# Optimization experiments

Hardware: AMD Instinct MI355X
Metric: run time of the kernel (lower is better)

## Reference

```python
import jax, jax.numpy as jnp
import numpy as np

B, S, D, L, V, H, FF = 128, 256, 512, 4, 96, 8, 512
DH = D // H
EPS = 1e-3  # keras BatchNormalization default epsilon


def setup_inputs() -> dict:
    key = jax.random.key(0)
    ks = jax.random.split(key, 12)
    s = 0.02
    inp = {
        "sequence": jax.random.randint(ks[0], (B, S), 0, V),
        "pos_encodings": jax.random.normal(ks[1], (S, D), jnp.float32) * s,
        "embed": jax.random.normal(ks[2], (V, D), jnp.float32) * s,
        "Wq": jax.random.normal(ks[3], (L, D, D), jnp.float32) * s,
        "bq": jnp.zeros((L, D), jnp.float32),
        "Wk": jax.random.normal(ks[4], (L, D, D), jnp.float32) * s,
        "bk": jnp.zeros((L, D), jnp.float32),
        "Wv": jax.random.normal(ks[5], (L, D, D), jnp.float32) * s,
        "bv": jnp.zeros((L, D), jnp.float32),
        "Wo": jax.random.normal(ks[6], (L, D, D), jnp.float32) * s,
        "bo": jnp.zeros((L, D), jnp.float32),
        "gamma1": jnp.ones((L, D), jnp.float32),
        "beta1": jnp.zeros((L, D), jnp.float32),
        "W1": jax.random.normal(ks[7], (L, D, FF), jnp.float32) * s,
        "b1": jnp.zeros((L, FF), jnp.float32),
        "W2": jax.random.normal(ks[8], (L, FF, D), jnp.float32) * s,
        "b2": jnp.zeros((L, D), jnp.float32),
        "gamma2": jnp.ones((L, D), jnp.float32),
        "beta2": jnp.zeros((L, D), jnp.float32),
    }
    return inp


def _batchnorm(h, g, b):
    # training-mode BN over (batch, seq) per feature, eps=1e-3
    mu = jnp.mean(h, axis=(0, 1), keepdims=True)
    var = jnp.mean(jnp.square(h - mu), axis=(0, 1), keepdims=True)
    return (h - mu) * jax.lax.rsqrt(var + EPS) * g + b


def _encoder(sequence, pos_encodings, embed, layer_params):
    x = embed[sequence] + pos_encodings[None]  # [B,S,D]

    def layer(h, p):
        wq, bq_, wk, bk_, wv, bv_, wo, bo_, g1, be1, w1, bb1, w2, bb2, g2, be2 = p
        b_, s_, d_ = h.shape
        q = (h @ wq + bq_).reshape(b_, s_, H, DH)
        k = (h @ wk + bk_).reshape(b_, s_, H, DH)
        v = (h @ wv + bv_).reshape(b_, s_, H, DH)
        scores = jnp.einsum('bqhd,bkhd->bhqk', q, k) / jnp.sqrt(jnp.float32(DH))
        attn = jnp.einsum('bhqk,bkhd->bqhd', jax.nn.softmax(scores, axis=-1), v)
        attn = attn.reshape(b_, s_, d_) @ wo + bo_
        h = _batchnorm(h + attn, g1, be1)
        ffn = jax.nn.relu(h @ w1 + bb1) @ w2 + bb2
        h = _batchnorm(h + ffn, g2, be2)
        return h, None

    out, _ = jax.lax.scan(layer, x, layer_params)
    return out


def reference(sequence, pos_encodings, embed, Wq, bq, Wk, bk, Wv, bv, Wo, bo,
              gamma1, beta1, W1, b1, W2, b2, gamma2, beta2):
    layer_params = (Wq, bq, Wk, bk, Wv, bv, Wo, bo,
                    gamma1, beta1, W1, b1, W2, b2, gamma2, beta2)
    return _encoder(sequence, pos_encodings, embed, layer_params)
```

## Files before the change

### kernel.cpp

```cpp
#include <hip/hip_runtime.h>

#define B_   128
#define S_   256
#define D_   512
#define L_   4
#define H_   8
#define DH_  64
#define FF_  512
#define M_   32768
#define EPS_ 1e-3f

typedef unsigned short u16;
typedef unsigned int   u32;
typedef __bf16 bf16_8 __attribute__((ext_vector_type(8)));
typedef float  f32_4  __attribute__((ext_vector_type(4)));

__device__ __forceinline__ float bf2f(u16 u) {
  union { u32 i; float f; } x; x.i = ((u32)u) << 16; return x.f;
}
__device__ __forceinline__ u16 f2bf(float f) {
  union { float f; u32 i; } x; x.f = f;
  u32 r = x.i + 0x7fffu + ((x.i >> 16) & 1u);
  return (u16)(r >> 16);
}
__device__ __forceinline__ void async_cp16(const void* g, void* l) {
  __builtin_amdgcn_global_load_lds(
      (const __attribute__((address_space(1))) void*)g,
      (__attribute__((address_space(3))) void*)l, 16, 0, 0);
}

__global__ __launch_bounds__(256) void k_embed(const int* __restrict__ seq,
    const float* __restrict__ pos, const float* __restrict__ emb,
    u16* __restrict__ h)
{
  int t = blockIdx.x * 256 + threadIdx.x;
  int row = t >> 6;
  int c = (t & 63) * 8;
  int s = row & (S_ - 1);
  int tok = seq[row];
  const float* ep = emb + (size_t)tok * D_ + c;
  const float* pp = pos + (size_t)s * D_ + c;
  float4 e0 = *(const float4*)ep;
  float4 e1 = *(const float4*)(ep + 4);
  float4 p0 = *(const float4*)pp;
  float4 p1 = *(const float4*)(pp + 4);
  u32 o[4];
  o[0] = (u32)f2bf(e0.x + p0.x) | ((u32)f2bf(e0.y + p0.y) << 16);
  o[1] = (u32)f2bf(e0.z + p0.z) | ((u32)f2bf(e0.w + p0.w) << 16);
  o[2] = (u32)f2bf(e1.x + p1.x) | ((u32)f2bf(e1.y + p1.y) << 16);
  o[3] = (u32)f2bf(e1.z + p1.z) | ((u32)f2bf(e1.w + p1.w) << 16);
  *(uint4*)&h[(size_t)row * D_ + c] = make_uint4(o[0], o[1], o[2], o[3]);
}

__global__ __launch_bounds__(256) void k_transpose(
    const float* __restrict__ Wq, const float* __restrict__ Wk, const float* __restrict__ Wv,
    const float* __restrict__ Wo, const float* __restrict__ W1, const float* __restrict__ W2,
    u16* __restrict__ Wt)
{
  __shared__ u16 tile[32][33];
  int mat = blockIdx.z;
  int layer = mat / 6, w = mat % 6;
  const float* src = (w == 0) ? Wq : (w == 1) ? Wk : (w == 2) ? Wv
                   : (w == 3) ? Wo : (w == 4) ? W1 : W2;
  src += (size_t)layer * (D_ * D_);
  u16* dst = Wt + (size_t)mat * (D_ * D_);
  int bx = blockIdx.x * 32;
  int by = blockIdx.y * 32;
  int tx = threadIdx.x & 31, ty = threadIdx.x >> 5;
#pragma unroll
  for (int i = 0; i < 32; i += 8)
    tile[ty + i][tx] = f2bf(src[(size_t)(by + ty + i) * D_ + bx + tx]);
  __syncthreads();
#pragma unroll
  for (int i = 0; i < 32; i += 8)
    dst[(size_t)(bx + ty + i) * D_ + by + tx] = tile[tx][ty + i];
}

__global__ __launch_bounds__(256) void k_packbias(const float* __restrict__ bq,
    const float* __restrict__ bk, const float* __restrict__ bv, float* __restrict__ dst)
{
  int t = blockIdx.x * 256 + threadIdx.x;
  int l = t / 1536, j = t - l * 1536;
  const float* src = (j < 512) ? bq : (j < 1024) ? bk : bv;
  dst[t] = src[l * 512 + (j & 511)];
}

__global__ __launch_bounds__(256) void k_gemm(
    const u16* __restrict__ A, const u16* __restrict__ Bt,
    const float* __restrict__ bias, const u16* __restrict__ resid,
    u16* __restrict__ outb, float* __restrict__ stats,
    int mode)
{
  __shared__ __align__(16) u16 smem[24576];
  u16* As = smem;
  u16* Bs = smem + 12288;
  int tid = threadIdx.x;
  int m0 = blockIdx.y * 128;
  int n0 = blockIdx.x * 128;
  int w = tid >> 6, lane = tid & 63;
  int wm = (w >> 1) * 64, wn = (w & 1) * 64;
  int fr = lane & 15, lk = lane >> 4;

  int srow = lane >> 2;
  int schunk = (lane & 3) ^ ((lane >> 4) & 3);
  const u16* Ag0 = A  + (size_t)(m0 + w * 32 + srow) * 512 + schunk * 8;
  const u16* Ag1 = Ag0 + (size_t)16 * 512;
  const u16* Bg0 = Bt + (size_t)(n0 + w * 32 + srow) * 512 + schunk * 8;
  const u16* Bg1 = Bg0 + (size_t)16 * 512;
  int off0 = (w * 32) * 32;
  int off1 = (w * 32 + 16) * 32;

  f32_4 acc[4][4] = {};
  int ach = (lk ^ ((fr >> 2) & 3)) * 8;

  async_cp16(Ag0, &As[off0]);
  async_cp16(Ag1, &As[off1]);
  async_cp16(Bg0, &Bs[off0]);
  async_cp16(Bg1, &Bs[off1]);
  async_cp16(Ag0 + 32, &As[4096 + off0]);
  async_cp16(Ag1 + 32, &As[4096 + off1]);
  async_cp16(Bg0 + 32, &Bs[4096 + off0]);
  async_cp16(Bg1 + 32, &Bs[4096 + off1]);

#pragma unroll
  for (int it = 0; it < 16; it++) {
    if (it < 15) asm volatile("s_waitcnt vmcnt(4)" ::: "memory");
    else         asm volatile("s_waitcnt vmcnt(0)" ::: "memory");
    __builtin_amdgcn_s_barrier();
    asm volatile("" ::: "memory");
    if (it < 14) {
      int kn = (it + 2) * 32;
      int pn = ((it + 2) % 3) * 4096;
      async_cp16(Ag0 + kn, &As[pn + off0]);
      async_cp16(Ag1 + kn, &As[pn + off1]);
      async_cp16(Bg0 + kn, &Bs[pn + off0]);
      async_cp16(Bg1 + kn, &Bs[pn + off1]);
    }
    const u16* Ab = &As[(it % 3) * 4096];
    const u16* Bb = &Bs[(it % 3) * 4096];
    bf16_8 afr[4], bfr[4];
#pragma unroll
    for (int i = 0; i < 4; i++) {
      afr[i] = *(const bf16_8*)&Ab[(wm + i * 16 + fr) * 32 + ach];
      bfr[i] = *(const bf16_8*)&Bb[(wn + i * 16 + fr) * 32 + ach];
    }
#pragma unroll
    for (int i = 0; i < 4; i++)
#pragma unroll
      for (int j = 0; j < 4; j++)
        acc[i][j] = __builtin_amdgcn_mfma_f32_16x16x32_bf16(afr[i], bfr[j], acc[i][j], 0, 0, 0);
  }

  __syncthreads();
  u16* Ct = smem;
  int rbase = lk * 4;
#pragma unroll
  for (int j = 0; j < 4; j++) {
    int colin = wn + j * 16 + fr;
    int colg  = n0 + colin;
    float bv = bias[colg];
    float csum = 0.f, csq = 0.f;
#pragma unroll
    for (int i = 0; i < 4; i++) {
      int rowl = wm + i * 16 + rbase;
#pragma unroll
      for (int r = 0; r < 4; r++) {
        float c = acc[i][j][r] + bv;
        if (mode == 1) c = fmaxf(c, 0.f);
        if (mode == 2) {
          c += bf2f(resid[(size_t)(m0 + rowl + r) * 512 + colg]);
          csum += c; csq = fmaf(c, c, csq);
        }
        int rw = rowl + r;
        Ct[rw * 128 + (((colin >> 3) ^ (rw & 15)) << 3) + (colin & 7)] = f2bf(c);
      }
    }
    if (mode == 2) {
      csum += __shfl_xor(csum, 16); csum += __shfl_xor(csum, 32);
      csq  += __shfl_xor(csq, 16);  csq  += __shfl_xor(csq, 32);
      if (lk == 0) {
        atomicAdd(&stats[colg], csum);
        atomicAdd(&stats[512 + colg], csq);
      }
    }
  }
  __syncthreads();

#pragma unroll
  for (int rd = 0; rd < 8; rd++) {
    int lrow = w * 32 + rd * 4 + (lane >> 4);
    int s = lane & 15;
    uint4 val = *(const uint4*)&Ct[lrow * 128 + s * 8];
    int chunk = s ^ (lrow & 15);
    int grow = m0 + lrow;
    if (mode == 3) {
      int colg = n0 + chunk * 8;
      int cc = colg & 511;
      size_t idx = (size_t)(colg >> 9) * ((size_t)M_ * D_)
                 + ((size_t)((grow >> 8) * 8 + (cc >> 6)) * 256 + (grow & 255)) * 64 + (cc & 63);
      *(uint4*)&outb[idx] = val;
    } else {
      *(uint4*)&outb[(size_t)grow * 512 + n0 + chunk * 8] = val;
    }
  }
}

__global__ __launch_bounds__(256) void k_attn(
    const u16* __restrict__ q, const u16* __restrict__ k,
    const u16* __restrict__ v, u16* __restrict__ attn)
{
  __shared__ u16 Vt[64 * 256];
  __shared__ u16 Pm[4][16 * 64];
  int tid = threadIdx.x;
  int h = blockIdx.x & 7, b = blockIdx.x >> 3;
  size_t hb = (size_t)(b * 8 + h) * (256 * 64);
  int w = tid >> 6, lane = tid & 63;

  {
    int kp = tid & 127;
    int o  = tid >> 7;
    const u16* vp = v + hb + (size_t)(2 * kp) * 64 + o * 32;
    union { uint4 u[4]; u16 s[32]; } r0, r1;
#pragma unroll
    for (int i = 0; i < 4; i++) {
      r0.u[i] = *(const uint4*)(vp + i * 8);
      r1.u[i] = *(const uint4*)(vp + 64 + i * 8);
    }
#pragma unroll
    for (int d = 0; d < 32; d++) {
      int da = o * 32 + d;
      u32 val = (u32)r0.s[d] | ((u32)r1.s[d] << 16);
      int idx = da * 256 + ((((kp >> 2) ^ (da & 31)) << 3)) + ((2 * kp) & 7);
      *(u32*)&Vt[idx] = val;
    }
  }
  __syncthreads();

  int fr = lane & 15;
  int lk = lane >> 4;
  int rbase = lk * 4;
  const u16* kb = k + hb;

#pragma unroll 1
  for (int qt = 0; qt < 4; qt++) {
    int q0 = qt * 64 + w * 16;

    f32_4 accS[16];
    const u16* qbase = q + hb + (size_t)(q0 + fr) * 64 + lk * 8;
    bf16_8 af0 = *(const bf16_8*)(qbase);
    bf16_8 af1 = *(const bf16_8*)(qbase + 32);
    __builtin_amdgcn_s_setprio(1);
#pragma unroll
    for (int j = 0; j < 16; j++) {
      const u16* kr = kb + (size_t)(j * 16 + fr) * 64;
      bf16_8 bf0 = *(const bf16_8*)(kr + lk * 8);
      bf16_8 bf1 = *(const bf16_8*)(kr + 32 + lk * 8);
      f32_4 z = {};
      z = __builtin_amdgcn_mfma_f32_16x16x32_bf16(af0, bf0, z, 0, 0, 0);
      accS[j] = __builtin_amdgcn_mfma_f32_16x16x32_bf16(af1, bf1, z, 0, 0, 0);
    }
    __builtin_amdgcn_s_setprio(0);

    float l[4];
#pragma unroll
    for (int r = 0; r < 4; r++) {
      float m = accS[0][r];
#pragma unroll
      for (int j = 1; j < 16; j++) m = fmaxf(m, accS[j][r]);
      m = fmaxf(m, __shfl_xor(m, 1));
      m = fmaxf(m, __shfl_xor(m, 2));
      m = fmaxf(m, __shfl_xor(m, 4));
      m = fmaxf(m, __shfl_xor(m, 8));
      float s = 0.f;
#pragma unroll
      for (int j = 0; j < 16; j++) {
        float p = __expf((accS[j][r] - m) * 0.125f);
        accS[j][r] = p;
        s += p;
      }
      s += __shfl_xor(s, 1);
      s += __shfl_xor(s, 2);
      s += __shfl_xor(s, 4);
      s += __shfl_xor(s, 8);
      l[r] = s;
    }

    f32_4 accO[4] = {};
#pragma unroll
    for (int hs = 0; hs < 4; hs++) {
#pragma unroll
      for (int j4 = 0; j4 < 4; j4++) {
        int col = j4 * 16 + fr;
        int ch = col >> 3, cl = col & 7;
#pragma unroll
        for (int r = 0; r < 4; r++) {
          int row = rbase + r;
          Pm[w][row * 64 + ((ch ^ (row & 7)) << 3) + cl] = f2bf(accS[hs * 4 + j4][r]);
        }
      }
      __builtin_amdgcn_s_setprio(1);
#pragma unroll
      for (int kk = 0; kk < 2; kk++) {
        bf16_8 pa = *(const bf16_8*)&Pm[w][fr * 64 + (((kk * 4 + lk) ^ (fr & 7)) << 3)];
#pragma unroll
        for (int jd = 0; jd < 4; jd++) {
          int brow = jd * 16 + fr;
          int ck = hs * 8 + kk * 4 + lk;
          bf16_8 vb = *(const bf16_8*)&Vt[brow * 256 + ((ck ^ (brow & 31)) << 3)];
          accO[jd] = __builtin_amdgcn_mfma_f32_16x16x32_bf16(pa, vb, accO[jd], 0, 0, 0);
        }
      }
      __builtin_amdgcn_s_setprio(0);
    }

    float linv[4];
#pragma unroll
    for (int r = 0; r < 4; r++) linv[r] = 1.f / l[r];
    size_t orow0 = (size_t)(b * S_ + q0 + rbase);
#pragma unroll
    for (int jd = 0; jd < 4; jd++) {
      int col = h * DH_ + jd * 16 + fr;
#pragma unroll
      for (int r = 0; r < 4; r++)
        attn[(orow0 + r) * D_ + col] = f2bf(accO[jd][r] * linv[r]);
    }
  }
}

__global__ __launch_bounds__(256) void k_zero(float* p, int n) {
  int t = blockIdx.x * 256 + threadIdx.x;
  if (t < n) p[t] = 0.f;
}

__global__ __launch_bounds__(256) void k_bnapply(const u16* __restrict__ P,
    const float* __restrict__ stats, const float* __restrict__ gamma,
    const float* __restrict__ beta, u16* __restrict__ outb, float* __restrict__ outf)
{
  size_t t8 = ((size_t)blockIdx.x * 256 + threadIdx.x) * 8;
  int f = (int)(t8 & 511);
  const float inv = 1.f / 32768.f;
  float sc[8], sh[8];
#pragma unroll
  for (int i = 0; i < 8; i++) {
    float mu = stats[f + i] * inv;
    float var = stats[512 + f + i] * inv - mu * mu;
    sc[i] = gamma[f + i] * rsqrtf(var + EPS_);
    sh[i] = beta[f + i] - mu * sc[i];
  }
  union { uint4 u; u16 s[8]; } pv;
  pv.u = *(const uint4*)&P[t8];
  float o[8];
#pragma unroll
  for (int i = 0; i < 8; i++) o[i] = bf2f(pv.s[i]) * sc[i] + sh[i];
  if (outf) {
    *(float4*)&outf[t8]     = make_float4(o[0], o[1], o[2], o[3]);
    *(float4*)&outf[t8 + 4] = make_float4(o[4], o[5], o[6], o[7]);
  } else {
    u32 u[4];
#pragma unroll
    for (int i = 0; i < 4; i++)
      u[i] = (u32)f2bf(o[2 * i]) | ((u32)f2bf(o[2 * i + 1]) << 16);
    *(uint4*)&outb[t8] = make_uint4(u[0], u[1], u[2], u[3]);
  }
}

extern "C" void kernel_launch(void* const* d_in, const int* in_sizes, int n_in,
                              void* d_out, int out_size, void* d_ws, size_t ws_size,
                              hipStream_t stream)
{
  const int*   seq = (const int*)d_in[0];
  const float* pos = (const float*)d_in[1];
  const float* emb = (const float*)d_in[2];
  const float* Wq  = (const float*)d_in[3];
  const float* bq  = (const float*)d_in[4];
  const float* Wk  = (const float*)d_in[5];
  const float* bk  = (const float*)d_in[6];
  const float* Wv  = (const float*)d_in[7];
  const float* bv  = (const float*)d_in[8];
  const float* Wo  = (const float*)d_in[9];
  const float* bo  = (const float*)d_in[10];
  const float* g1  = (const float*)d_in[11];
  const float* be1 = (const float*)d_in[12];
  const float* W1  = (const float*)d_in[13];
  const float* b1  = (const float*)d_in[14];
  const float* W2  = (const float*)d_in[15];
  const float* b2  = (const float*)d_in[16];
  const float* g2  = (const float*)d_in[17];
  const float* be2 = (const float*)d_in[18];

  char* ws = (char*)d_ws;
  const size_t SZH = (size_t)M_ * D_ * 2;
  u16* hb16 = (u16*)(ws);
  u16* qB   = (u16*)(ws + SZH);
  u16* kB   = (u16*)(ws + 2 * SZH);
  u16* vB   = (u16*)(ws + 3 * SZH);
  u16* aB   = (u16*)(ws + 4 * SZH);
  u16* PB   = (u16*)(ws + 2 * SZH);
  u16* tB   = qB;
  u16* Wt   = (u16*)(ws + 5 * SZH);
  float* stats = (float*)(ws + 5 * SZH + (size_t)24 * D_ * D_ * 2);
  float* bqkv  = stats + 8192;

  dim3 blk(256);
  k_zero<<<32, blk, 0, stream>>>(stats, 8192);
  k_packbias<<<24, blk, 0, stream>>>(bq, bk, bv, bqkv);
  k_transpose<<<dim3(16, 16, 24), blk, 0, stream>>>(Wq, Wk, Wv, Wo, W1, W2, Wt);
  k_embed<<<M_ * 64 / 256, blk, 0, stream>>>(seq, pos, emb, hb16);

  dim3 ggrid(512 / 128, M_ / 128);
  dim3 qgrid(1536 / 128, M_ / 128);
  for (int l = 0; l < L_; l++) {
    const u16* wtqkv = Wt + (size_t)(l * 6 + 0) * D_ * D_;
    const u16* wto = Wt + (size_t)(l * 6 + 3) * D_ * D_;
    const u16* wt1 = Wt + (size_t)(l * 6 + 4) * D_ * D_;
    const u16* wt2 = Wt + (size_t)(l * 6 + 5) * D_ * D_;
    float* st = stats + l * 2048;

    k_gemm<<<qgrid, blk, 0, stream>>>(hb16, wtqkv, bqkv + l * 1536, nullptr, qB, nullptr, 3);
    k_attn<<<B_ * H_, blk, 0, stream>>>(qB, kB, vB, aB);
    k_gemm<<<ggrid, blk, 0, stream>>>(aB, wto, bo + l * D_, hb16, PB, st, 2);
    k_bnapply<<<8192, blk, 0, stream>>>(PB, st, g1 + l * D_, be1 + l * D_, hb16, nullptr);
    k_gemm<<<ggrid, blk, 0, stream>>>(hb16, wt1, b1 + l * FF_, nullptr, tB, nullptr, 1);
    k_gemm<<<ggrid, blk, 0, stream>>>(tB, wt2, b2 + l * D_, hb16, PB, st + 1024, 2);
    if (l == L_ - 1)
      k_bnapply<<<8192, blk, 0, stream>>>(PB, st + 1024, g2 + l * D_, be2 + l * D_, nullptr, (float*)d_out);
    else
      k_bnapply<<<8192, blk, 0, stream>>>(PB, st + 1024, g2 + l * D_, be2 + l * D_, hb16, nullptr);
  }
}
```

Before: 1.535 ms.

## Enlarge GEMM tile to 256x256 with 512-thread blocks and two-pass epilogue

Doubles the GEMM block tile from 128x128 to 256x256, using 8 waves that each compute a 128x64 sub-tile with 8x4 MFMA accumulators. Each loaded A/B element is reused more, which cuts global and LDS traffic per flop. The epilogue now stages the output through LDS in two 128-row passes so the staging buffer fits. In exchange the kernel uses 96KB of LDS and about 128 accumulator VGPRs per thread, and the grid has fewer blocks (256 or 768), so occupancy and load balance across CUs may drop.

```diff
diff --git a/kernel.cpp b/kernel.cpp
--- a/kernel.cpp
+++ b/kernel.cpp
@@ -85,20 +85,21 @@
   dst[t] = src[l * 512 + (j & 511)];
 }
 
-__global__ __launch_bounds__(256) void k_gemm(
+__global__ __launch_bounds__(512) void k_gemm(
     const u16* __restrict__ A, const u16* __restrict__ Bt,
     const float* __restrict__ bias, const u16* __restrict__ resid,
     u16* __restrict__ outb, float* __restrict__ stats,
     int mode)
 {
-  __shared__ __align__(16) u16 smem[24576];
+  __shared__ __align__(16) u16 smem[49152];
   u16* As = smem;
-  u16* Bs = smem + 12288;
+  u16* Bs = smem + 24576;
   int tid = threadIdx.x;
-  int m0 = blockIdx.y * 128;
-  int n0 = blockIdx.x * 128;
+  int m0 = blockIdx.y * 256;
+  int n0 = blockIdx.x * 256;
   int w = tid >> 6, lane = tid & 63;
-  int wm = (w >> 1) * 64, wn = (w & 1) * 64;
+  int wr = w >> 2, wc = w & 3;
+  int wm = wr * 128, wn = wc * 64;
   int fr = lane & 15, lk = lane >> 4;
 
   int srow = lane >> 2;
@@ -107,20 +108,20 @@
   const u16* Ag1 = Ag0 + (size_t)16 * 512;
   const u16* Bg0 = Bt + (size_t)(n0 + w * 32 + srow) * 512 + schunk * 8;
   const u16* Bg1 = Bg0 + (size_t)16 * 512;
-  int off0 = (w * 32) * 32;
-  int off1 = (w * 32 + 16) * 32;
-
-  f32_4 acc[4][4] = {};
+  int off0 = w * 1024;
+  int off1 = off0 + 512;
+
+  f32_4 acc[8][4] = {};
   int ach = (lk ^ ((fr >> 2) & 3)) * 8;
 
   async_cp16(Ag0, &As[off0]);
   async_cp16(Ag1, &As[off1]);
   async_cp16(Bg0, &Bs[off0]);
   async_cp16(Bg1, &Bs[off1]);
-  async_cp16(Ag0 + 32, &As[4096 + off0]);
-  async_cp16(Ag1 + 32, &As[4096 + off1]);
-  async_cp16(Bg0 + 32, &Bs[4096 + off0]);
-  async_cp16(Bg1 + 32, &Bs[4096 + off1]);
+  async_cp16(Ag0 + 32, &As[8192 + off0]);
+  async_cp16(Ag1 + 32, &As[8192 + off1]);
+  async_cp16(Bg0 + 32, &Bs[8192 + off0]);
+  async_cp16(Bg1 + 32, &Bs[8192 + off1]);
 
 #pragma unroll
   for (int it = 0; it < 16; it++) {
@@ -130,22 +131,23 @@
     asm volatile("" ::: "memory");
     if (it < 14) {
       int kn = (it + 2) * 32;
-      int pn = ((it + 2) % 3) * 4096;
+      int pn = ((it + 2) % 3) * 8192;
       async_cp16(Ag0 + kn, &As[pn + off0]);
       async_cp16(Ag1 + kn, &As[pn + off1]);
       async_cp16(Bg0 + kn, &Bs[pn + off0]);
       async_cp16(Bg1 + kn, &Bs[pn + off1]);
     }
-    const u16* Ab = &As[(it % 3) * 4096];
-    const u16* Bb = &Bs[(it % 3) * 4096];
-    bf16_8 afr[4], bfr[4];
-#pragma unroll
-    for (int i = 0; i < 4; i++) {
+    const u16* Ab = &As[(it % 3) * 8192];
+    const u16* Bb = &Bs[(it % 3) * 8192];
+    bf16_8 afr[8], bfr[4];
+#pragma unroll
+    for (int i = 0; i < 8; i++)
       afr[i] = *(const bf16_8*)&Ab[(wm + i * 16 + fr) * 32 + ach];
-      bfr[i] = *(const bf16_8*)&Bb[(wn + i * 16 + fr) * 32 + ach];
-    }
-#pragma unroll
-    for (int i = 0; i < 4; i++)
+#pragma unroll
+    for (int j = 0; j < 4; j++)
+      bfr[j] = *(const bf16_8*)&Bb[(wn + j * 16 + fr) * 32 + ach];
+#pragma unroll
+    for (int i = 0; i < 8; i++)
 #pragma unroll
       for (int j = 0; j < 4; j++)
         acc[i][j] = __builtin_amdgcn_mfma_f32_16x16x32_bf16(afr[i], bfr[j], acc[i][j], 0, 0, 0);
@@ -154,54 +156,60 @@
   __syncthreads();
   u16* Ct = smem;
   int rbase = lk * 4;
-#pragma unroll
-  for (int j = 0; j < 4; j++) {
-    int colin = wn + j * 16 + fr;
-    int colg  = n0 + colin;
-    float bv = bias[colg];
-    float csum = 0.f, csq = 0.f;
-#pragma unroll
-    for (int i = 0; i < 4; i++) {
-      int rowl = wm + i * 16 + rbase;
-#pragma unroll
-      for (int r = 0; r < 4; r++) {
-        float c = acc[i][j][r] + bv;
-        if (mode == 1) c = fmaxf(c, 0.f);
+#pragma unroll 1
+  for (int pass = 0; pass < 2; pass++) {
+    if (wr == pass) {
+#pragma unroll
+      for (int j = 0; j < 4; j++) {
+        int colin = wn + j * 16 + fr;
+        int colg  = n0 + colin;
+        float bv = bias[colg];
+        float csum = 0.f, csq = 0.f;
+#pragma unroll
+        for (int i = 0; i < 8; i++) {
+          int rowp = i * 16 + rbase;
+          int rowg = m0 + wm + rowp;
+#pragma unroll
+          for (int r = 0; r < 4; r++) {
+            float c = acc[i][j][r] + bv;
+            if (mode == 1) c = fmaxf(c, 0.f);
+            if (mode == 2) {
+              c += bf2f(resid[(size_t)(rowg + r) * 512 + colg]);
+              csum += c; csq = fmaf(c, c, csq);
+            }
+            int rw = rowp + r;
+            Ct[rw * 256 + (((colin >> 3) ^ (rw & 15)) << 3) + (colin & 7)] = f2bf(c);
+          }
+        }
         if (mode == 2) {
-          c += bf2f(resid[(size_t)(m0 + rowl + r) * 512 + colg]);
-          csum += c; csq = fmaf(c, c, csq);
+          csum += __shfl_xor(csum, 16); csum += __shfl_xor(csum, 32);
+          csq  += __shfl_xor(csq, 16);  csq  += __shfl_xor(csq, 32);
+          if (lk == 0) {
+            atomicAdd(&stats[colg], csum);
+            atomicAdd(&stats[512 + colg], csq);
+          }
         }
-        int rw = rowl + r;
-        Ct[rw * 128 + (((colin >> 3) ^ (rw & 15)) << 3) + (colin & 7)] = f2bf(c);
       }
     }
-    if (mode == 2) {
-      csum += __shfl_xor(csum, 16); csum += __shfl_xor(csum, 32);
-      csq  += __shfl_xor(csq, 16);  csq  += __shfl_xor(csq, 32);
-      if (lk == 0) {
-        atomicAdd(&stats[colg], csum);
-        atomicAdd(&stats[512 + colg], csq);
+    __syncthreads();
+#pragma unroll
+    for (int rd = 0; rd < 8; rd++) {
+      int lrow = w * 16 + rd * 2 + (lane >> 5);
+      int s = lane & 31;
+      uint4 val = *(const uint4*)&Ct[lrow * 256 + s * 8];
+      int chunk = s ^ (lrow & 15);
+      int grow = m0 + pass * 128 + lrow;
+      if (mode == 3) {
+        int colg = n0 + chunk * 8;
+        int cc = colg & 511;
+        size_t idx = (size_t)(colg >> 9) * ((size_t)M_ * D_)
+                   + ((size_t)((grow >> 8) * 8 + (cc >> 6)) * 256 + (grow & 255)) * 64 + (cc & 63);
+        *(uint4*)&outb[idx] = val;
+      } else {
+        *(uint4*)&outb[(size_t)grow * 512 + n0 + chunk * 8] = val;
       }
     }
-  }
-  __syncthreads();
-
-#pragma unroll
-  for (int rd = 0; rd < 8; rd++) {
-    int lrow = w * 32 + rd * 4 + (lane >> 4);
-    int s = lane & 15;
-    uint4 val = *(const uint4*)&Ct[lrow * 128 + s * 8];
-    int chunk = s ^ (lrow & 15);
-    int grow = m0 + lrow;
-    if (mode == 3) {
-      int colg = n0 + chunk * 8;
-      int cc = colg & 511;
-      size_t idx = (size_t)(colg >> 9) * ((size_t)M_ * D_)
-                 + ((size_t)((grow >> 8) * 8 + (cc >> 6)) * 256 + (grow & 255)) * 64 + (cc & 63);
-      *(uint4*)&outb[idx] = val;
-    } else {
-      *(uint4*)&outb[(size_t)grow * 512 + n0 + chunk * 8] = val;
-    }
+    __syncthreads();
   }
 }
 
@@ -402,13 +410,14 @@
   float* bqkv  = stats + 8192;
 
   dim3 blk(256);
+  dim3 gblk(512);
   k_zero<<<32, blk, 0, stream>>>(stats, 8192);
   k_packbias<<<24, blk, 0, stream>>>(bq, bk, bv, bqkv);
   k_transpose<<<dim3(16, 16, 24), blk, 0, stream>>>(Wq, Wk, Wv, Wo, W1, W2, Wt);
   k_embed<<<M_ * 64 / 256, blk, 0, stream>>>(seq, pos, emb, hb16);
 
-  dim3 ggrid(512 / 128, M_ / 128);
-  dim3 qgrid(1536 / 128, M_ / 128);
+  dim3 ggrid(512 / 256, M_ / 256);
+  dim3 qgrid(1536 / 256, M_ / 256);
   for (int l = 0; l < L_; l++) {
     const u16* wtqkv = Wt + (size_t)(l * 6 + 0) * D_ * D_;
     const u16* wto = Wt + (size_t)(l * 6 + 3) * D_ * D_;
@@ -416,12 +425,12 @@
     const u16* wt2 = Wt + (size_t)(l * 6 + 5) * D_ * D_;
     float* st = stats + l * 2048;
 
-    k_gemm<<<qgrid, blk, 0, stream>>>(hb16, wtqkv, bqkv + l * 1536, nullptr, qB, nullptr, 3);
+    k_gemm<<<qgrid, gblk, 0, stream>>>(hb16, wtqkv, bqkv + l * 1536, nullptr, qB, nullptr, 3);
     k_attn<<<B_ * H_, blk, 0, stream>>>(qB, kB, vB, aB);
-    k_gemm<<<ggrid, blk, 0, stream>>>(aB, wto, bo + l * D_, hb16, PB, st, 2);
+    k_gemm<<<ggrid, gblk, 0, stream>>>(aB, wto, bo + l * D_, hb16, PB, st, 2);
     k_bnapply<<<8192, blk, 0, stream>>>(PB, st, g1 + l * D_, be1 + l * D_, hb16, nullptr);
-    k_gemm<<<ggrid, blk, 0, stream>>>(hb16, wt1, b1 + l * FF_, nullptr, tB, nullptr, 1);
-    k_gemm<<<ggrid, blk, 0, stream>>>(tB, wt2, b2 + l * D_, hb16, PB, st + 1024, 2);
+    k_gemm<<<ggrid, gblk, 0, stream>>>(hb16, wt1, b1 + l * FF_, nullptr, tB, nullptr, 1);
+    k_gemm<<<ggrid, gblk, 0, stream>>>(tB, wt2, b2 + l * D_, hb16, PB, st + 1024, 2);
     if (l == L_ - 1)
       k_bnapply<<<8192, blk, 0, stream>>>(PB, st + 1024, g2 + l * D_, be2 + l * D_, nullptr, (float*)d_out);
     else
```

Result: slower. 3.935 ms (+156.4%).
